# Performance work log

Measured on AMD Instinct MI355X. Metric: run time of the kernel, lower is better.

## Reference

```python
import jax, jax.numpy as jnp
import numpy as np

MIN_FP16 = float(np.finfo(np.float16).min)  # -65504.0, matches torch.finfo(torch.float16).min


def _apply_rotary(x, cos, sin):
    # x: [B, H, S, D]; cos/sin: [S, D//2]
    # Equivalent to view_as_complex on interleaved pairs, multiply by freq_cis, view_as_real.
    xr = x[..., 0::2]
    xi = x[..., 1::2]
    c = cos[None, None]  # [1,1,S,D//2]
    s = sin[None, None]
    out_r = xr * c - xi * s
    out_i = xr * s + xi * c
    return jnp.stack([out_r, out_i], axis=-1).reshape(x.shape)


def setup_inputs() -> dict:
    key = jax.random.key(0)
    ks = jax.random.split(key, 4)
    B, S, D_MODEL, H = 2, 2048, 1024, 16
    HS = D_MODEL // H  # 64
    x = jax.random.normal(ks[0], (B, S, D_MODEL), dtype=jnp.float32)
    # Standard RoPE frequencies: theta_i = 10000^(-2i/HS)
    inv_freq = 1.0 / (10000.0 ** (np.arange(0, HS, 2, dtype=np.float32) / HS))  # [HS//2]
    t = np.arange(S, dtype=np.float32)
    angles = np.outer(t, inv_freq)  # [S, HS//2]
    cos = jnp.asarray(np.cos(angles))
    sin = jnp.asarray(np.sin(angles))
    mask = jnp.tril(jnp.ones((S, S), dtype=jnp.int32))[None, None]  # [1,1,S,S] causal
    scale = 1.0 / np.sqrt(D_MODEL)
    W_proj = jax.random.normal(ks[1], (D_MODEL, 3 * D_MODEL), dtype=jnp.float32) * scale
    b_proj = jnp.zeros((3 * D_MODEL,), dtype=jnp.float32)
    W_ff = jax.random.normal(ks[2], (D_MODEL, D_MODEL), dtype=jnp.float32) * scale
    b_ff = jnp.zeros((D_MODEL,), dtype=jnp.float32)
    return {"x": x, "cos_q": cos, "sin_q": sin, "cos_k": cos, "sin_k": sin,
            "mask": mask, "W_proj": W_proj, "b_proj": b_proj, "W_ff": W_ff, "b_ff": b_ff}


def reference(x, cos_q, sin_q, cos_k, sin_k, mask, W_proj, b_proj, W_ff, b_ff):
    B, S, d_model = x.shape
    H = 16
    HS = d_model // H
    head_scale = jnp.sqrt(jnp.float32(HS))

    # fused QKV projection, then split: [B,S,3*dm] -> [3,B,H,S,HS]
    x_proj = x @ W_proj + b_proj
    x_proj = x_proj.reshape(B, S, 3, H, HS).transpose(2, 0, 3, 1, 4)
    q, k, v = x_proj[0], x_proj[1], x_proj[2]

    # mask path: cache pre-RoPE k,v
    next_prefix_kv = jnp.stack([k, v])  # [2,B,H,S,HS]

    q = _apply_rotary(q, cos_q, sin_q)
    k = _apply_rotary(k, cos_k, sin_k)

    scores = jnp.einsum('bhqd,bhkd->bhqk', q, k) / head_scale
    scores = jnp.where(mask == 0, jnp.float32(MIN_FP16), scores)
    probs = jax.nn.softmax(scores, axis=-1)
    attn_o = jnp.einsum('bhqk,bhkd->bhqd', probs, v)  # [B,H,S,HS]

    attn_o = attn_o.transpose(0, 2, 1, 3).reshape(B, S, d_model)
    ff_o = attn_o @ W_ff + b_ff
    return ff_o, next_prefix_kv
```

## Files before the change

### kernel.cpp

```cpp
#include <hip/hip_runtime.h>
#include <stdint.h>

#define DM    1024
#define NH    16
#define HS    64
#define S_LEN 2048

typedef short bf16x8 __attribute__((ext_vector_type(8)));
typedef float f32x4  __attribute__((ext_vector_type(4)));
typedef unsigned short u16x4 __attribute__((ext_vector_type(4)));

__device__ __forceinline__ uint16_t f2b(float f) {
    union { float f; uint32_t i; } x; x.f = f;
    uint32_t r = x.i + 0x7fffu + ((x.i >> 16) & 1u);
    return (uint16_t)(r >> 16);
}
__device__ __forceinline__ uint32_t pack2(float a, float b) {
    return (uint32_t)f2b(a) | ((uint32_t)f2b(b) << 16);
}
__device__ __forceinline__ f32x4 mfma16(bf16x8 a, bf16x8 b, f32x4 c) {
    return __builtin_amdgcn_mfma_f32_16x16x32_bf16(a, b, c, 0, 0, 0);
}
template<int CTRL>
__device__ __forceinline__ float dpp_max(float x) {
    union { float f; int i; } u; u.f = x;
    int y = __builtin_amdgcn_update_dpp(u.i, u.i, CTRL, 0xF, 0xF, true);
    union { int i; float f; } v; v.i = y;
    return fmaxf(x, v.f);
}

__global__ __launch_bounds__(256) void convert_bf16(
    const float* __restrict__ in, uint16_t* __restrict__ out)
{
    const size_t i = (size_t)blockIdx.x * 256 + threadIdx.x;
    const float4* p = (const float4*)in + i * 2;
    float4 a = p[0], b = p[1];
    uint4 o;
    o.x = pack2(a.x, a.y); o.y = pack2(a.z, a.w);
    o.z = pack2(b.x, b.y); o.w = pack2(b.z, b.w);
    ((uint4*)out)[i] = o;
}

__global__ __launch_bounds__(256) void transpose_w(
    const float* __restrict__ W, uint16_t* __restrict__ WT, int N)
{
    __shared__ float T[32][33];
    const int tx = threadIdx.x & 31, ty = threadIdx.x >> 5;
    const int n0 = blockIdx.x * 32, k0 = blockIdx.y * 32;
    #pragma unroll
    for (int i = 0; i < 4; ++i)
        T[ty + i * 8][tx] = W[(size_t)(k0 + ty + i * 8) * N + n0 + tx];
    __syncthreads();
    #pragma unroll
    for (int i = 0; i < 4; ++i)
        WT[(size_t)(n0 + ty + i * 8) * 1024 + k0 + tx] = f2b(T[tx][ty + i * 8]);
}

template<int MODE, bool ABF, bool WV>
__global__ __launch_bounds__(256) void gemm_mfma(
    const void* __restrict__ Araw,
    const uint16_t* __restrict__ BT,
    const float* __restrict__ bias,
    int N,
    const float* __restrict__ cq, const float* __restrict__ sq,
    const float* __restrict__ ck, const float* __restrict__ sk,
    uint16_t* __restrict__ qbuf, uint16_t* __restrict__ kbuf,
    float* __restrict__ kout, float* __restrict__ vout,
    uint16_t* __restrict__ vtb,
    float* __restrict__ Cout)
{
    __shared__ uint16_t As[128][40];
    __shared__ uint16_t Bs[128][40];

    const int tid  = threadIdx.x;
    const int wave = tid >> 6, lane = tid & 63;
    const int quad = lane >> 4, li = lane & 15;
    const int wm = (wave >> 1) * 64, wn = (wave & 1) * 64;
    const int m0 = blockIdx.y * 128, n0 = blockIdx.x * 128;

    f32x4 acc[4][4];
    #pragma unroll
    for (int a = 0; a < 4; ++a)
        #pragma unroll
        for (int c = 0; c < 4; ++c)
            acc[a][c] = (f32x4){0.f, 0.f, 0.f, 0.f};

    const int sm = tid >> 1, skc = (tid & 1) * 16;

    uint4 aw0, aw1, bw0, bw1;
    auto load_k = [&](int k0) {
        if (ABF) {
            const uint16_t* ap = (const uint16_t*)Araw + (size_t)(m0 + sm) * 1024 + k0 + skc;
            aw0 = *(const uint4*)ap;
            aw1 = *(const uint4*)(ap + 8);
        } else {
            const float* ap = (const float*)Araw + (size_t)(m0 + sm) * 1024 + k0 + skc;
            float4 f0 = *(const float4*)(ap + 0),  f1 = *(const float4*)(ap + 4);
            float4 f2 = *(const float4*)(ap + 8),  f3 = *(const float4*)(ap + 12);
            aw0.x = pack2(f0.x, f0.y); aw0.y = pack2(f0.z, f0.w);
            aw0.z = pack2(f1.x, f1.y); aw0.w = pack2(f1.z, f1.w);
            aw1.x = pack2(f2.x, f2.y); aw1.y = pack2(f2.z, f2.w);
            aw1.z = pack2(f3.x, f3.y); aw1.w = pack2(f3.z, f3.w);
        }
        const uint16_t* bp = BT + (size_t)(n0 + sm) * 1024 + k0 + skc;
        bw0 = *(const uint4*)bp;
        bw1 = *(const uint4*)(bp + 8);
    };

    load_k(0);
    for (int k0 = 0; k0 < 1024; k0 += 32) {
        __syncthreads();
        *(uint4*)&As[sm][skc]     = aw0;
        *(uint4*)&As[sm][skc + 8] = aw1;
        *(uint4*)&Bs[sm][skc]     = bw0;
        *(uint4*)&Bs[sm][skc + 8] = bw1;
        __syncthreads();
        if (k0 + 32 < 1024) load_k(k0 + 32);

        bf16x8 af[4], bf[4];
        #pragma unroll
        for (int mi = 0; mi < 4; ++mi)
            af[mi] = *(const bf16x8*)&As[wm + mi * 16 + li][quad * 8];
        #pragma unroll
        for (int ni = 0; ni < 4; ++ni)
            bf[ni] = *(const bf16x8*)&Bs[wn + ni * 16 + li][quad * 8];
        #pragma unroll
        for (int mi = 0; mi < 4; ++mi)
            #pragma unroll
            for (int ni = 0; ni < 4; ++ni)
                acc[mi][ni] = mfma16(af[mi], bf[ni], acc[mi][ni]);
    }

    if (MODE == 1) {
        #pragma unroll
        for (int ni = 0; ni < 4; ++ni) {
            const int n = n0 + wn + ni * 16 + li;
            const float bb = bias[n];
            #pragma unroll
            for (int mi = 0; mi < 4; ++mi)
                #pragma unroll
                for (int r = 0; r < 4; ++r) {
                    const int m = m0 + wm + mi * 16 + quad * 4 + r;
                    Cout[(size_t)m * N + n] = acc[mi][ni][r] + bb;
                }
        }
    } else {
        #pragma unroll
        for (int ni = 0; ni < 4; ++ni) {
            const int n   = n0 + wn + ni * 16 + li;
            const int sel = n >> 10;
            const int d   = n & 1023;
            const int h   = d >> 6;
            const int hd  = d & 63;
            const int i0  = hd >> 1;
            const float bb = bias[n];
            #pragma unroll
            for (int mi = 0; mi < 4; ++mi) {
                const int mb = m0 + wm + mi * 16 + quad * 4;
                const int b  = mb >> 11;
                const int s0 = mb & 2047;
                float vv[4];
                #pragma unroll
                for (int r = 0; r < 4; ++r) {
                    const int s = s0 + r;
                    const float val  = acc[mi][ni][r] + bb;
                    const float part = __shfl_xor(val, 1);
                    const size_t idx = ((size_t)(b * NH + h) * S_LEN + s) * HS + hd;
                    if (sel == 0) {
                        float c = cq[s * 32 + i0], sn = sq[s * 32 + i0];
                        float o = (hd & 1) ? (part * sn + val * c) : (val * c - part * sn);
                        qbuf[idx] = f2b(o * 0.125f);
                    } else if (sel == 1) {
                        kout[idx] = val;
                        float c = ck[s * 32 + i0], sn = sk[s * 32 + i0];
                        float o = (hd & 1) ? (part * sn + val * c) : (val * c - part * sn);
                        kbuf[idx] = f2b(o);
                    } else {
                        vout[idx] = val;
                        vv[r] = val;
                    }
                }
                if (WV && sel == 2) {
                    u16x4 u;
                    u[0] = f2b(vv[0]); u[1] = f2b(vv[1]);
                    u[2] = f2b(vv[2]); u[3] = f2b(vv[3]);
                    *(u16x4*)&vtb[((size_t)(b * NH + h) * HS + hd) * S_LEN + s0] = u;
                }
            }
        }
    }
}

__global__ __launch_bounds__(256) void attn_mfma(
    const uint16_t* __restrict__ qbuf,
    const uint16_t* __restrict__ kbuf,
    const uint16_t* __restrict__ vtb,
    uint16_t* __restrict__ obuf)
{
    __shared__ uint16_t Ks[64][72];
    __shared__ uint16_t Vt[64][72];
    __shared__ uint16_t Ps[64][68];

    const int i  = blockIdx.x;
    const int bh = i >> 5;
    const int jj = i & 31;
    const int g  = jj >> 3, cc = jj & 7;
    const int qt = (g == 0) ? (31 - cc) : (g == 1) ? cc : (g == 2) ? (23 - cc) : (8 + cc);
    const int h = bh & 15, b = bh >> 4;
    const int tid = threadIdx.x;
    const int wave = tid >> 6, lane = tid & 63;
    const int quad = lane >> 4, li = lane & 15;
    const int wrow0 = wave * 16;

    const short onebf = (short)0x3F80;
    const bf16x8 kOnes = {onebf, onebf, onebf, onebf, onebf, onebf, onebf, onebf};

    const uint16_t* qp = qbuf + ((size_t)bh * S_LEN + qt * 64 + wrow0 + li) * HS + quad * 8;
    const bf16x8 aq0 = *(const bf16x8*)qp;
    const bf16x8 aq1 = *(const bf16x8*)(qp + 32);

    f32x4 oacc[4];
    float m_i[4], l_i[4];
    #pragma unroll
    for (int r = 0; r < 4; ++r) {
        m_i[r] = -1e30f; l_i[r] = 0.f;
        oacc[r] = (f32x4){0.f, 0.f, 0.f, 0.f};
    }

    const int row = tid >> 2, c = (tid & 3) * 16;
    uint4 kr0, kr1, vr0, vr1;

    auto load_kv = [&](int kt) {
        const uint16_t* kp = kbuf + ((size_t)bh * S_LEN + kt * 64 + row) * HS + c;
        kr0 = *(const uint4*)kp;
        kr1 = *(const uint4*)(kp + 8);
        const uint16_t* vp = vtb + ((size_t)bh * HS + row) * S_LEN + kt * 64 + c;
        vr0 = *(const uint4*)vp;
        vr1 = *(const uint4*)(vp + 8);
    };
    load_kv(0);

    for (int kt = 0; kt <= qt; ++kt) {
        __syncthreads();
        *(uint4*)&Ks[row][c]     = kr0;
        *(uint4*)&Ks[row][c + 8] = kr1;
        *(uint4*)&Vt[row][c]     = vr0;
        *(uint4*)&Vt[row][c + 8] = vr1;
        __syncthreads();
        if (kt < qt) load_kv(kt + 1);

        f32x4 sacc[4];
        __builtin_amdgcn_s_setprio(1);
        #pragma unroll
        for (int ni = 0; ni < 4; ++ni) {
            bf16x8 b0 = *(const bf16x8*)&Ks[ni * 16 + li][quad * 8];
            bf16x8 b1 = *(const bf16x8*)&Ks[ni * 16 + li][32 + quad * 8];
            f32x4 z = (f32x4){0.f, 0.f, 0.f, 0.f};
            z = mfma16(aq0, b0, z);
            sacc[ni] = mfma16(aq1, b1, z);
        }
        __builtin_amdgcn_s_setprio(0);

        const bool diag = (kt == qt);
        float p[4][4];
        #pragma unroll
        for (int ni = 0; ni < 4; ++ni)
            #pragma unroll
            for (int r = 0; r < 4; ++r) {
                float v = sacc[ni][r];
                if (diag && (ni * 16 + li > wrow0 + quad * 4 + r)) v = -65504.f;
                p[ni][r] = v;
            }
        float alp[4];
        #pragma unroll
        for (int r = 0; r < 4; ++r) {
            float mx = fmaxf(fmaxf(p[0][r], p[1][r]), fmaxf(p[2][r], p[3][r]));
            mx = dpp_max<0xB1>(mx);
            mx = dpp_max<0x4E>(mx);
            mx = dpp_max<0x124>(mx);
            mx = dpp_max<0x128>(mx);
            float mnew  = fmaxf(m_i[r], mx);
            alp[r] = __expf(m_i[r] - mnew);
            m_i[r] = mnew;
            #pragma unroll
            for (int ni = 0; ni < 4; ++ni)
                p[ni][r] = __expf(p[ni][r] - mnew);
            #pragma unroll
            for (int ni = 0; ni < 4; ++ni) oacc[ni][r] *= alp[r];
        }

        #pragma unroll
        for (int ni = 0; ni < 4; ++ni)
            #pragma unroll
            for (int r = 0; r < 4; ++r)
                Ps[wrow0 + quad * 4 + r][ni * 16 + li] = f2b(p[ni][r]);

        bf16x8 pa0 = *(const bf16x8*)&Ps[wrow0 + li][quad * 8];
        bf16x8 pa1 = *(const bf16x8*)&Ps[wrow0 + li][32 + quad * 8];

        __builtin_amdgcn_s_setprio(1);
        f32x4 ls = (f32x4){0.f, 0.f, 0.f, 0.f};
        ls = mfma16(pa0, kOnes, ls);
        ls = mfma16(pa1, kOnes, ls);

        #pragma unroll
        for (int ni = 0; ni < 4; ++ni) {
            bf16x8 v0 = *(const bf16x8*)&Vt[ni * 16 + li][quad * 8];
            bf16x8 v1 = *(const bf16x8*)&Vt[ni * 16 + li][32 + quad * 8];
            oacc[ni] = mfma16(pa0, v0, oacc[ni]);
            oacc[ni] = mfma16(pa1, v1, oacc[ni]);
        }
        __builtin_amdgcn_s_setprio(0);

        #pragma unroll
        for (int r = 0; r < 4; ++r)
            l_i[r] = l_i[r] * alp[r] + ls[r];
    }

    #pragma unroll
    for (int ni = 0; ni < 4; ++ni)
        #pragma unroll
        for (int r = 0; r < 4; ++r) {
            const int qg = qt * 64 + wrow0 + quad * 4 + r;
            obuf[((size_t)b * S_LEN + qg) * DM + h * HS + ni * 16 + li] =
                f2b(oacc[ni][r] / l_i[r]);
        }
}

extern "C" void kernel_launch(void* const* d_in, const int* in_sizes, int n_in,
                              void* d_out, int out_size, void* d_ws, size_t ws_size,
                              hipStream_t stream) {
    const float* x  = (const float*)d_in[0];
    const float* cq = (const float*)d_in[1];
    const float* sq = (const float*)d_in[2];
    const float* ck = (const float*)d_in[3];
    const float* sk = (const float*)d_in[4];
    const float* Wp = (const float*)d_in[6];
    const float* bp = (const float*)d_in[7];
    const float* Wf = (const float*)d_in[8];
    const float* bf = (const float*)d_in[9];

    float* out  = (float*)d_out;
    float* ffo  = out;
    float* kout = out + 4194304;
    float* vout = out + 8388608;

    uint16_t* qbuf = (uint16_t*)d_ws;
    uint16_t* kbuf = qbuf + 4194304;
    uint16_t* abuf = kbuf + 4194304;
    uint16_t* vtb  = abuf + 4194304;
    uint16_t* xbf  = vtb  + 4194304;
    uint16_t* WpT  = abuf;
    uint16_t* WfT  = qbuf;

    const bool has_xbf = ws_size >= (size_t)40 * 1024 * 1024;

    dim3 blk(256);
    transpose_w<<<dim3(96, 32), blk, 0, stream>>>(Wp, WpT, 3072);
    if (has_xbf) {
        convert_bf16<<<dim3(2048), blk, 0, stream>>>(x, xbf);
        gemm_mfma<0, true, true><<<dim3(24, 32), blk, 0, stream>>>(
            xbf, WpT, bp, 3072, cq, sq, ck, sk,
            qbuf, kbuf, kout, vout, vtb, nullptr);
    } else {
        gemm_mfma<0, false, true><<<dim3(24, 32), blk, 0, stream>>>(
            x, WpT, bp, 3072, cq, sq, ck, sk,
            qbuf, kbuf, kout, vout, vtb, nullptr);
    }
    attn_mfma<<<dim3(1024), blk, 0, stream>>>(qbuf, kbuf, vtb, abuf);
    transpose_w<<<dim3(32, 32), blk, 0, stream>>>(Wf, WfT, 1024);
    gemm_mfma<1, true, false><<<dim3(8, 32), blk, 0, stream>>>(
        abuf, WfT, bf, 1024, nullptr, nullptr, nullptr, nullptr,
        nullptr, nullptr, nullptr, nullptr, nullptr, ffo);
}
```

Measured before the change: 300.8 us.

## Double-buffer LDS tiles in MFMA GEMM to halve barriers per k-step

Converts the GEMM main loop from single-buffered shared memory with two barriers per 32-wide k-step to a ping-pong scheme with two LDS buffers and register prefetch two steps ahead. Each k-step now needs only one barrier, and the store of the next tile overlaps with MFMA work on the current buffer. The cost is doubled LDS use per block and more live registers for two sets of prefetched tiles, which could lower occupancy.

```diff
diff --git a/kernel.cpp b/kernel.cpp
--- a/kernel.cpp
+++ b/kernel.cpp
@@ -69,8 +69,8 @@
     uint16_t* __restrict__ vtb,
     float* __restrict__ Cout)
 {
-    __shared__ uint16_t As[128][40];
-    __shared__ uint16_t Bs[128][40];
+    __shared__ uint16_t As[2][128][40];
+    __shared__ uint16_t Bs[2][128][40];
 
     const int tid  = threadIdx.x;
     const int wave = tid >> 6, lane = tid & 63;
@@ -87,48 +87,64 @@
 
     const int sm = tid >> 1, skc = (tid & 1) * 16;
 
-    uint4 aw0, aw1, bw0, bw1;
-    auto load_k = [&](int k0) {
+    uint4 a0[2], b0[2], a1[2], b1[2];
+
+    auto loadk = [&](int K0, uint4 (&AW)[2], uint4 (&BW)[2]) {
         if (ABF) {
-            const uint16_t* ap = (const uint16_t*)Araw + (size_t)(m0 + sm) * 1024 + k0 + skc;
-            aw0 = *(const uint4*)ap;
-            aw1 = *(const uint4*)(ap + 8);
+            const uint16_t* ap = (const uint16_t*)Araw + (size_t)(m0 + sm) * 1024 + K0 + skc;
+            AW[0] = *(const uint4*)ap;
+            AW[1] = *(const uint4*)(ap + 8);
         } else {
-            const float* ap = (const float*)Araw + (size_t)(m0 + sm) * 1024 + k0 + skc;
+            const float* ap = (const float*)Araw + (size_t)(m0 + sm) * 1024 + K0 + skc;
             float4 f0 = *(const float4*)(ap + 0),  f1 = *(const float4*)(ap + 4);
             float4 f2 = *(const float4*)(ap + 8),  f3 = *(const float4*)(ap + 12);
-            aw0.x = pack2(f0.x, f0.y); aw0.y = pack2(f0.z, f0.w);
-            aw0.z = pack2(f1.x, f1.y); aw0.w = pack2(f1.z, f1.w);
-            aw1.x = pack2(f2.x, f2.y); aw1.y = pack2(f2.z, f2.w);
-            aw1.z = pack2(f3.x, f3.y); aw1.w = pack2(f3.z, f3.w);
-        }
-        const uint16_t* bp = BT + (size_t)(n0 + sm) * 1024 + k0 + skc;
-        bw0 = *(const uint4*)bp;
-        bw1 = *(const uint4*)(bp + 8);
+            AW[0].x = pack2(f0.x, f0.y); AW[0].y = pack2(f0.z, f0.w);
+            AW[0].z = pack2(f1.x, f1.y); AW[0].w = pack2(f1.z, f1.w);
+            AW[1].x = pack2(f2.x, f2.y); AW[1].y = pack2(f2.z, f2.w);
+            AW[1].z = pack2(f3.x, f3.y); AW[1].w = pack2(f3.z, f3.w);
+        }
+        const uint16_t* bp = BT + (size_t)(n0 + sm) * 1024 + K0 + skc;
+        BW[0] = *(const uint4*)bp;
+        BW[1] = *(const uint4*)(bp + 8);
     };
-
-    load_k(0);
-    for (int k0 = 0; k0 < 1024; k0 += 32) {
+    auto store = [&](int BUF, const uint4 (&AW)[2], const uint4 (&BW)[2]) {
+        *(uint4*)&As[BUF][sm][skc]     = AW[0];
+        *(uint4*)&As[BUF][sm][skc + 8] = AW[1];
+        *(uint4*)&Bs[BUF][sm][skc]     = BW[0];
+        *(uint4*)&Bs[BUF][sm][skc + 8] = BW[1];
+    };
+    auto compute = [&](int BUF) {
+        bf16x8 af[4], bfr[4];
+        #pragma unroll
+        for (int mi = 0; mi < 4; ++mi)
+            af[mi] = *(const bf16x8*)&As[BUF][wm + mi * 16 + li][quad * 8];
+        #pragma unroll
+        for (int ni = 0; ni < 4; ++ni)
+            bfr[ni] = *(const bf16x8*)&Bs[BUF][wn + ni * 16 + li][quad * 8];
+        #pragma unroll
+        for (int mi = 0; mi < 4; ++mi)
+            #pragma unroll
+            for (int ni = 0; ni < 4; ++ni)
+                acc[mi][ni] = mfma16(af[mi], bfr[ni], acc[mi][ni]);
+    };
+
+    loadk(0, a0, b0);
+    store(0, a0, b0);
+    loadk(32, a1, b1);
+    __syncthreads();
+
+    for (int t = 0; t < 32; t += 2) {
+        const int kb = t * 32;
+        if (kb + 64 < 1024) loadk(kb + 64, a0, b0);
+        compute(0);
+        store(1, a1, b1);
         __syncthreads();
-        *(uint4*)&As[sm][skc]     = aw0;
-        *(uint4*)&As[sm][skc + 8] = aw1;
-        *(uint4*)&Bs[sm][skc]     = bw0;
-        *(uint4*)&Bs[sm][skc + 8] = bw1;
-        __syncthreads();
-        if (k0 + 32 < 1024) load_k(k0 + 32);
-
-        bf16x8 af[4], bf[4];
-        #pragma unroll
-        for (int mi = 0; mi < 4; ++mi)
-            af[mi] = *(const bf16x8*)&As[wm + mi * 16 + li][quad * 8];
-        #pragma unroll
-        for (int ni = 0; ni < 4; ++ni)
-            bf[ni] = *(const bf16x8*)&Bs[wn + ni * 16 + li][quad * 8];
-        #pragma unroll
-        for (int mi = 0; mi < 4; ++mi)
-            #pragma unroll
-            for (int ni = 0; ni < 4; ++ni)
-                acc[mi][ni] = mfma16(af[mi], bf[ni], acc[mi][ni]);
+        if (kb + 96 < 1024) loadk(kb + 96, a1, b1);
+        compute(1);
+        if (kb + 64 < 1024) {
+            store(0, a0, b0);
+            __syncthreads();
+        }
     }
 
     if (MODE == 1) {
```

New measurement: 434.9 us. +44.6%, slower.
